# Kernel optimization log

Hardware: AMD Instinct MI355X
Metric: run time of the kernel (lower is better)

The kernel has to match this reference:

```python
import jax, jax.numpy as jnp
import numpy as np

N_NODES = 100000
N_EDGES = 3200000


def setup_inputs() -> dict:
    key = jax.random.key(0)
    ks = jax.random.split(key, 12)
    x = jax.random.normal(ks[0], (N_NODES, 5), dtype=jnp.float32)
    edges = jax.random.randint(ks[1], (2, N_EDGES), 0, N_NODES)
    edge_attr = jax.random.normal(ks[2], (N_EDGES, 2), dtype=jnp.float32)
    detector_labels = jax.random.bernoulli(ks[3], 0.7, (N_NODES,))

    def init(k, shape, fan_in):
        return (jax.random.normal(k, shape, dtype=jnp.float32) / np.sqrt(fan_in)).astype(jnp.float32)

    W_gat = init(ks[4], (5, 16), 5)        # GATConv lin (shared src/dst)
    att_src = init(ks[5], (16,), 16)
    att_dst = init(ks[6], (16,), 16)
    W_edge = init(ks[7], (2, 16), 2)       # GATConv lin_edge
    att_edge = init(ks[8], (16,), 16)
    b_gat = jnp.zeros((16,), jnp.float32)
    W1 = init(ks[9], (34, 64), 34)
    b1 = jnp.zeros((64,), jnp.float32)
    W2 = init(ks[10], (64, 2), 64)
    b2 = jnp.zeros((2,), jnp.float32)
    return dict(x=x, edges=edges, edge_attr=edge_attr, detector_labels=detector_labels,
                W_gat=W_gat, att_src=att_src, att_dst=att_dst, W_edge=W_edge,
                att_edge=att_edge, b_gat=b_gat, W1=W1, b1=b1, W2=W2, b2=b2)


def reference(x, edges, edge_attr, detector_labels, W_gat, att_src, att_dst,
              W_edge, att_edge, b_gat, W1, b1, W2, b2):
    n_nodes = x.shape[0]
    src, dst = edges[0], edges[1]

    # --- GATConv(5 -> 16, heads=1, concat=False, edge_dim=2, no self loops) ---
    h = x @ W_gat                                        # [N, 16]
    a_src = h @ att_src                                  # [N]
    a_dst = h @ att_dst                                  # [N]
    a_edge = (edge_attr @ W_edge) @ att_edge             # [E]
    alpha = jax.nn.leaky_relu(a_src[src] + a_dst[dst] + a_edge, 0.2)
    # segmented softmax over incoming edges of each dst node
    seg_max = jax.ops.segment_max(alpha, dst, num_segments=n_nodes)
    ex = jnp.exp(alpha - seg_max[dst])
    denom = jax.ops.segment_sum(ex, dst, num_segments=n_nodes)
    a = ex / (denom[dst] + 1e-16)                        # [E]
    out = jax.ops.segment_sum(h[src] * a[:, None], dst, num_segments=n_nodes) + b_gat
    xh = jax.nn.relu(out)                                # [N, 16]

    # --- edge update: gather-concat-MLP ---
    feat = jnp.concatenate([xh[src], edge_attr, xh[dst]], axis=-1)   # [E, 34]
    ef = jax.nn.relu(feat @ W1 + b1) @ W2 + b2                       # [E, 2]

    # --- SplitSyndromes: keep edges whose both endpoints are detectors ---
    valid = detector_labels[src] & detector_labels[dst]
    idx = jnp.nonzero(valid)[0]        # eager (data-dependent size, not jitted)
    return edges[:, idx], jax.nn.sigmoid(ef[idx])
```

## Files before the change

kernel.cpp:

```cpp
#include <hip/hip_runtime.h>

#define NN 100000
#define NE 3200000
#define CH 8192
#define NCB ((NE + CH - 1) / CH)
#define THR 1024
#define ITH (CH / THR)
#define NBK ((NN + 63) >> 6)
#define CAP 2560
#define NWG (NE / 64)
#define NSTRIP 8
#define SLEN ((NCB + NSTRIP - 1) / NSTRIP)

typedef __attribute__((ext_vector_type(8))) __bf16 bf16x8;
typedef __attribute__((ext_vector_type(4))) float f32x4;

union BF8 { unsigned short u[8]; bf16x8 v; };

__global__ void kdetect(const unsigned char* __restrict__ lab8, int* __restrict__ flags) {
  __shared__ int tmp[256];
  int t = threadIdx.x;
  int s = 0;
  for (int i = t; i < 25000; i += 256) s += lab8[4 * i + 1];
  tmp[t] = s;
  __syncthreads();
  for (int d = 128; d > 0; d >>= 1) { if (t < d) tmp[t] += tmp[t + d]; __syncthreads(); }
  if (t == 0) flags[0] = (tmp[0] != 0) ? 1 : 0;
}

__global__ void klab(const void* __restrict__ lab, const int* __restrict__ flags,
                     int* __restrict__ labN) {
  int n = blockIdx.x * 256 + threadIdx.x;
  if (n >= NN) return;
  int v;
  if (flags[0]) v = ((const unsigned char*)lab)[n];
  else          v = ((const int*)lab)[n];
  labN[n] = (v != 0) ? 1 : 0;
}

__global__ void kc01(const float* __restrict__ We, const float* __restrict__ ae,
                     float* __restrict__ c01) {
  if (threadIdx.x == 0) {
    float c0 = 0.f, c1 = 0.f;
    for (int k = 0; k < 16; k++) { c0 += We[k] * ae[k]; c1 += We[16 + k] * ae[k]; }
    c01[0] = c0; c01[1] = c1;
  }
}

__global__ void knodeA(const float* __restrict__ x, const float* __restrict__ Wg,
                       const float* __restrict__ atts, const float* __restrict__ attd,
                       const int* __restrict__ labN,
                       float2* __restrict__ pka, float2* __restrict__ pkd) {
  int n = blockIdx.x * 256 + threadIdx.x;
  if (n >= NN) return;
  float xi[5];
#pragma unroll
  for (int i = 0; i < 5; i++) xi[i] = x[n * 5 + i];
  float asum = 0.f, dsum = 0.f;
#pragma unroll
  for (int k = 0; k < 16; k++) {
    float acc = 0.f;
#pragma unroll
    for (int i = 0; i < 5; i++) acc += xi[i] * Wg[i * 16 + k];
    asum += acc * atts[k];
    dsum += acc * attd[k];
  }
  float lab = labN[n] ? 1.f : 0.f;
  pka[n] = make_float2(asum, lab);
  pkd[n] = make_float2(dsum, lab);
}

__global__ __launch_bounds__(THR) void khist(const int* __restrict__ src,
                                             const int* __restrict__ dst,
                                             const int* __restrict__ labN,
                                             int* __restrict__ blkcnt,
                                             int* __restrict__ cntw,
                                             int* __restrict__ cntc) {
  __shared__ int hist[NBK];
  __shared__ int vsum;
  int tid = threadIdx.x, b = blockIdx.x;
  for (int i = tid; i < NBK; i += THR) hist[i] = 0;
  if (tid == 0) vsum = 0;
  __syncthreads();
  int lane = tid & 63, wid = tid >> 6;
  int wsum = 0;
  for (int it = 0; it < ITH; ++it) {
    int e = b * CH + it * THR + tid;
    int v = 0;
    if (e < NE) {
      int s = src[e], d = dst[e];
      atomicAdd(&hist[d >> 6], 1);
      v = labN[s] & labN[d];
    }
    unsigned long long m = __ballot(v != 0);
    int c = __popcll(m);
    if (lane == 0) {
      int wg = b * (CH / 64) + it * 16 + wid;
      if (wg < NWG) cntw[wg] = c;
      wsum += c;
    }
  }
  if (lane == 0) atomicAdd(&vsum, wsum);
  __syncthreads();
  int* row = blkcnt + (size_t)b * NBK;
  for (int i = tid; i < NBK; i += THR) row[i] = hist[i];
  if (tid == 0) cntc[b] = vsum;
}

__global__ __launch_bounds__(256) void kscanc1(int* __restrict__ blkcnt,
                                               int* __restrict__ ssum) {
  int i = blockIdx.x * 256 + threadIdx.x;
  int st = blockIdx.y;
  if (i >= NBK) return;
  int c0 = st * SLEN, c1 = min(c0 + SLEN, NCB);
  int run = 0;
  for (int c = c0; c < c1; c++) {
    int* p = blkcnt + (size_t)c * NBK + i;
    int v = *p;
    *p = run;
    run += v;
  }
  ssum[st * NBK + i] = run;
}

__global__ __launch_bounds__(256) void kscanc2(int* __restrict__ ssum,
                                               int* __restrict__ total) {
  int i = blockIdx.x * 256 + threadIdx.x;
  if (i >= NBK) return;
  int run = 0;
#pragma unroll
  for (int st = 0; st < NSTRIP; st++) {
    int v = ssum[st * NBK + i];
    ssum[st * NBK + i] = run;
    run += v;
  }
  total[i] = run;
}

__global__ __launch_bounds__(256) void kaddbb(int* __restrict__ ssum,
                                              const int* __restrict__ bb) {
  int i = blockIdx.x * 256 + threadIdx.x;
  if (i >= NBK) return;
  int v = bb[i];
#pragma unroll
  for (int st = 0; st < NSTRIP; st++) ssum[st * NBK + i] += v;
}

__global__ void kscan(const int* __restrict__ cnt, int* __restrict__ off, int nb) {
  __shared__ int tmp[256];
  __shared__ int carry;
  int t = threadIdx.x;
  if (t == 0) carry = 0;
  __syncthreads();
  for (int base = 0; base < nb; base += 256) {
    int i = base + t;
    int v = (i < nb) ? cnt[i] : 0;
    tmp[t] = v;
    __syncthreads();
    for (int d = 1; d < 256; d <<= 1) {
      int add = (t >= d) ? tmp[t - d] : 0;
      __syncthreads();
      tmp[t] += add;
      __syncthreads();
    }
    if (i < nb) off[i] = carry + tmp[t] - v;
    __syncthreads();
    if (t == 0) carry += tmp[255];
    __syncthreads();
  }
  if (t == 0) off[nb] = carry;
}

__global__ __launch_bounds__(128) void kscanw(const int* __restrict__ cntw,
                                              const int* __restrict__ offc,
                                              int* __restrict__ offw) {
  int b = blockIdx.x, t = threadIdx.x;
  __shared__ int a[128];
  int wg = b * 128 + t;
  int val = (wg < NWG) ? cntw[wg] : 0;
  a[t] = val;
  __syncthreads();
  for (int d = 1; d < 128; d <<= 1) {
    int x = (t >= d) ? a[t - d] : 0;
    __syncthreads();
    a[t] += x;
    __syncthreads();
  }
  if (wg < NWG) offw[wg] = offc[b] + a[t] - val;
}

__global__ __launch_bounds__(THR) void kscat(
    const int* __restrict__ src, const int* __restrict__ dst,
    const float* __restrict__ eattr,
    const float2* __restrict__ pka, const float2* __restrict__ pkd,
    const float* __restrict__ c01,
    const int* __restrict__ blkcnt, const int* __restrict__ ssum,
    const int* __restrict__ offw,
    uint2* __restrict__ bins, float* __restrict__ out,
    float2* __restrict__ eat2, int NV) {
  __shared__ uint2 pay[CH];
  __shared__ unsigned short pbk[CH];
  __shared__ int hist[2048];
  __shared__ int ps[1024];
  __shared__ int lcur[2048];
  __shared__ int goff[NBK];
  int b = blockIdx.x, tid = threadIdx.x;
  for (int i = tid; i < 2048; i += THR) hist[i] = 0;
  float c0 = c01[0], c1 = c01[1];
  const int* bc = blkcnt + (size_t)b * NBK;
  const int* ss = ssum + (size_t)(b / SLEN) * NBK;
  __syncthreads();
  int lane = tid & 63, wid = tid >> 6;
  uint2 st[ITH];
  unsigned short sb[ITH];
#pragma unroll
  for (int it = 0; it < ITH; ++it) {
    int e = b * CH + it * THR + tid;
    int v = 0;
    int s = 0, d = 0;
    float2 ea;
    if (e < NE) {
      s = src[e]; d = dst[e];
      ea = ((const float2*)eattr)[e];
      float2 ga = pka[s], gd = pkd[d];
      float al = ga.x + gd.x + ea.x * c0 + ea.y * c1;
      al = (al > 0.f) ? al : 0.2f * al;
      float exv = __expf(al);
      int bk = d >> 6;
      atomicAdd(&hist[bk], 1);
      st[it].x = ((unsigned)s << 6) | (unsigned)(d & 63);
      st[it].y = __float_as_uint(exv);
      sb[it] = (unsigned short)bk;
      v = (ga.y != 0.f) && (gd.y != 0.f);
    } else {
      sb[it] = 0xffffu;
    }
    unsigned long long m = __ballot(v);
    if (v) {
      int wg = b * (CH / 64) + it * 16 + wid;
      int p = offw[wg] + __popcll(m & ((1ull << lane) - 1ull));
      if (p < NV) {
        out[p] = (float)s;
        out[NV + p] = (float)d;
        eat2[p] = ea;
      }
    }
  }
  __syncthreads();
  int h0 = hist[2 * tid], h1 = hist[2 * tid + 1];
  ps[tid] = h0 + h1;
  __syncthreads();
  for (int d = 1; d < 1024; d <<= 1) {
    int v = (tid >= d) ? ps[tid - d] : 0;
    __syncthreads();
    ps[tid] += v;
    __syncthreads();
  }
  int epair = (tid > 0) ? ps[tid - 1] : 0;
  int l0 = epair, l1 = epair + h0;
  lcur[2 * tid] = l0;
  lcur[2 * tid + 1] = l1;
  {
    int i0 = 2 * tid, i1 = 2 * tid + 1;
    if (i0 < NBK) goff[i0] = ss[i0] + bc[i0] - l0;
    if (i1 < NBK) goff[i1] = ss[i1] + bc[i1] - l1;
  }
  __syncthreads();
#pragma unroll
  for (int it = 0; it < ITH; ++it) {
    if (sb[it] != 0xffffu) {
      int pos = atomicAdd(&lcur[sb[it]], 1);
      pay[pos] = st[it];
      pbk[pos] = sb[it];
    }
  }
  __syncthreads();
  int n = ps[1023];
  for (int j = tid; j < n; j += THR) {
    int i = pbk[j];
    bins[goff[i] + j] = pay[j];
  }
}

__global__ __launch_bounds__(512) void kagg(
    const uint2* __restrict__ bins, const int* __restrict__ bucket_base,
    const float* __restrict__ x, const float* __restrict__ Wg,
    const float* __restrict__ bg, float* __restrict__ xh) {
  __shared__ uint2 pay[CAP];
  __shared__ int cnt[64], inc[64], cur[64];
  __shared__ float sWg[80], sbg[16];
  int k = blockIdx.x, tid = threadIdx.x;
  if (tid < 80) sWg[tid] = Wg[tid];
  else if (tid < 96) sbg[tid - 80] = bg[tid - 80];
  int start = bucket_base[k], end = bucket_base[k + 1];
  int node0 = k << 6;
  int c = tid & 15, g = tid >> 4;
  __syncthreads();
  float w0 = sWg[c], w1 = sWg[16 + c], w2 = sWg[32 + c], w3 = sWg[48 + c], w4 = sWg[64 + c];
  float acc[2] = {0.f, 0.f}, den[2] = {0.f, 0.f};
  for (int cb = start; cb < end; cb += CAP) {
    int n = min(end - cb, CAP);
    if (tid < 64) cnt[tid] = 0;
    __syncthreads();
    uint2 st0, st1, st2, st3, st4;
    {
      int i;
      i = tid;          if (i < n) { st0 = bins[cb + i]; atomicAdd(&cnt[st0.x & 63], 1); }
      i = tid + 512;    if (i < n) { st1 = bins[cb + i]; atomicAdd(&cnt[st1.x & 63], 1); }
      i = tid + 1024;   if (i < n) { st2 = bins[cb + i]; atomicAdd(&cnt[st2.x & 63], 1); }
      i = tid + 1536;   if (i < n) { st3 = bins[cb + i]; atomicAdd(&cnt[st3.x & 63], 1); }
      i = tid + 2048;   if (i < n) { st4 = bins[cb + i]; atomicAdd(&cnt[st4.x & 63], 1); }
    }
    __syncthreads();
    if (tid < 64) inc[tid] = cnt[tid];
    __syncthreads();
    for (int d = 1; d < 64; d <<= 1) {
      int v = 0;
      if (tid >= d && tid < 64) v = inc[tid - d];
      __syncthreads();
      if (tid < 64) inc[tid] += v;
      __syncthreads();
    }
    if (tid < 64) cur[tid] = inc[tid] - cnt[tid];
    __syncthreads();
    {
      int i;
      i = tid;          if (i < n) pay[atomicAdd(&cur[st0.x & 63], 1)] = st0;
      i = tid + 512;    if (i < n) pay[atomicAdd(&cur[st1.x & 63], 1)] = st1;
      i = tid + 1024;   if (i < n) pay[atomicAdd(&cur[st2.x & 63], 1)] = st2;
      i = tid + 1536;   if (i < n) pay[atomicAdd(&cur[st3.x & 63], 1)] = st3;
      i = tid + 2048;   if (i < n) pay[atomicAdd(&cur[st4.x & 63], 1)] = st4;
    }
    __syncthreads();
#pragma unroll
    for (int p = 0; p < 2; ++p) {
      int nd = p * 32 + g;
      int re = inc[nd], rs = re - cnt[nd];
      float a = 0.f, ds = 0.f;
      for (int idx = rs; idx < re; ++idx) {
        uint2 pl = pay[idx];
        int s = (int)(pl.x >> 6);
        float exv = __uint_as_float(pl.y);
        const float* xp = x + s * 5;
        float h = xp[0] * w0 + xp[1] * w1 + xp[2] * w2 + xp[3] * w3 + xp[4] * w4;
        a += h * exv;
        ds += exv;
      }
      acc[p] += a; den[p] += ds;
    }
    __syncthreads();
  }
#pragma unroll
  for (int p = 0; p < 2; ++p) {
    int node = node0 + p * 32 + g;
    if (node < NN) {
      float dn = fmaxf(den[p], 1e-30f);
      float v = acc[p] / dn + sbg[c];
      xh[node * 16 + c] = (v > 0.f) ? v : 0.f;
    }
  }
}

__global__ __launch_bounds__(256) void kmlp(
    const float2* __restrict__ eat2, const float* __restrict__ xh,
    const float* __restrict__ W1, const float* __restrict__ b1,
    const float* __restrict__ W2, const float* __restrict__ b2,
    float* __restrict__ out, int NV) {
  int tid = threadIdx.x;
  int lane = tid & 63, wid = tid >> 6;
  int lo4 = lane & 15, q = lane >> 4;

  BF8 bh[4], bl[4];
#pragma unroll
  for (int ct = 0; ct < 4; ct++) {
    int col = ct * 16 + lo4;
#pragma unroll
    for (int i = 0; i < 8; i++) {
      int k = q * 8 + i;
      int r = (k < 16) ? k : (k + 2);
      float w = W1[r * 64 + col];
      unsigned u = __float_as_uint(w);
      float rem = w - __uint_as_float(u & 0xffff0000u);
      bh[ct].u[i] = (unsigned short)(u >> 16);
      bl[ct].u[i] = (unsigned short)(__float_as_uint(rem) >> 16);
    }
  }
  float b1v[4], w16v[4], w17v[4], w2a[4], w2b[4];
#pragma unroll
  for (int ct = 0; ct < 4; ct++) {
    int j = ct * 16 + lo4;
    b1v[ct] = b1[j];
    w16v[ct] = W1[16 * 64 + j];
    w17v[ct] = W1[17 * 64 + j];
    w2a[ct] = W2[j * 2 + 0];
    w2b[ct] = W2[j * 2 + 1];
  }
  float bias20 = b2[0], bias21 = b2[1];

  int nwaves = gridDim.x * 4;
  int ntiles = (NV + 15) >> 4;
  for (int tb = blockIdx.x * 4 + wid; tb < ntiles; tb += nwaves) {
    int base = tb * 16;
    BF8 ah, al;
    {
      int p = base + lo4;
      float vals[8] = {0.f, 0.f, 0.f, 0.f, 0.f, 0.f, 0.f, 0.f};
      if (p < NV) {
        int node = (int)out[((q < 2) ? 0 : NV) + p];
        const float4* xp = (const float4*)(xh + node * 16 + (q & 1) * 8);
        float4 f0 = xp[0], f1 = xp[1];
        vals[0] = f0.x; vals[1] = f0.y; vals[2] = f0.z; vals[3] = f0.w;
        vals[4] = f1.x; vals[5] = f1.y; vals[6] = f1.z; vals[7] = f1.w;
      }
#pragma unroll
      for (int i = 0; i < 8; i++) {
        unsigned u = __float_as_uint(vals[i]);
        float rem = vals[i] - __uint_as_float(u & 0xffff0000u);
        ah.u[i] = (unsigned short)(u >> 16);
        al.u[i] = (unsigned short)(__float_as_uint(rem) >> 16);
      }
    }
    f32x4 acc[4];
#pragma unroll
    for (int ct = 0; ct < 4; ct++) {
      f32x4 z = {0.f, 0.f, 0.f, 0.f};
      z = __builtin_amdgcn_mfma_f32_16x16x32_bf16(ah.v, bh[ct].v, z, 0, 0, 0);
      z = __builtin_amdgcn_mfma_f32_16x16x32_bf16(ah.v, bl[ct].v, z, 0, 0, 0);
      z = __builtin_amdgcn_mfma_f32_16x16x32_bf16(al.v, bh[ct].v, z, 0, 0, 0);
      acc[ct] = z;
    }
    float o0[4], o1[4];
#pragma unroll
    for (int reg = 0; reg < 4; reg++) {
      int pr = base + q * 4 + reg;
      float2 ea = make_float2(0.f, 0.f);
      if (pr < NV) ea = eat2[pr];
      float s0 = 0.f, s1 = 0.f;
#pragma unroll
      for (int ct = 0; ct < 4; ct++) {
        float h = acc[ct][reg] + b1v[ct] + ea.x * w16v[ct] + ea.y * w17v[ct];
        h = fmaxf(h, 0.f);
        s0 += h * w2a[ct];
        s1 += h * w2b[ct];
      }
      o0[reg] = s0; o1[reg] = s1;
    }
#pragma unroll
    for (int m = 1; m < 16; m <<= 1) {
#pragma unroll
      for (int reg = 0; reg < 4; reg++) {
        o0[reg] += __shfl_xor(o0[reg], m, 64);
        o1[reg] += __shfl_xor(o1[reg], m, 64);
      }
    }
    if (lo4 == 0) {
#pragma unroll
      for (int reg = 0; reg < 4; reg++) {
        int pr = base + q * 4 + reg;
        if (pr < NV) {
          float v0 = bias20 + o0[reg], v1 = bias21 + o1[reg];
          ((float2*)(out + 2 * (size_t)NV))[pr] = make_float2(
              1.f / (1.f + __expf(-v0)), 1.f / (1.f + __expf(-v1)));
        }
      }
    }
  }
}

static inline size_t al64(size_t v) { return (v + 63) & ~(size_t)63; }

extern "C" void kernel_launch(void* const* d_in, const int* in_sizes, int n_in,
                              void* d_out, int out_size, void* d_ws, size_t ws_size,
                              hipStream_t stream) {
  const float* x     = (const float*)d_in[0];
  const int*   edges = (const int*)d_in[1];
  const float* eattr = (const float*)d_in[2];
  const void*  labels= d_in[3];
  const float* Wg    = (const float*)d_in[4];
  const float* atts  = (const float*)d_in[5];
  const float* attd  = (const float*)d_in[6];
  const float* We    = (const float*)d_in[7];
  const float* atte  = (const float*)d_in[8];
  const float* bg    = (const float*)d_in[9];
  const float* W1    = (const float*)d_in[10];
  const float* b1    = (const float*)d_in[11];
  const float* W2    = (const float*)d_in[12];
  const float* b2    = (const float*)d_in[13];
  float* out = (float*)d_out;
  const int NV = out_size / 4;
  const int* src = edges;
  const int* dst = edges + NE;

  char* w = (char*)d_ws;
  float* xh    = (float*)w;   w += al64((size_t)NN * 64);
  uint2* bins  = (uint2*)w;   w += al64((size_t)NE * 8);
  float2* eat2 = (float2*)w;  w += al64((size_t)NV * 8);
  float2* pka  = (float2*)w;  w += al64((size_t)NN * 8);
  float2* pkd  = (float2*)w;  w += al64((size_t)NN * 8);
  int* labN    = (int*)w;     w += al64((size_t)NN * 4);
  int* blkcnt  = (int*)w;     w += al64((size_t)NCB * NBK * 4);
  int* ssum    = (int*)w;     w += al64((size_t)NSTRIP * NBK * 4);
  int* total   = (int*)w;     w += al64((size_t)NBK * 4);
  int* bb      = (int*)w;     w += al64((size_t)(NBK + 1) * 4);
  int* cntc    = (int*)w;     w += al64((size_t)NCB * 4);
  int* offc    = (int*)w;     w += al64((size_t)(NCB + 1) * 4);
  int* cntw    = (int*)w;     w += al64((size_t)NWG * 4);
  int* offw    = (int*)w;     w += al64((size_t)NWG * 4);
  float* c01   = (float*)w;   w += 64;
  int* flags   = (int*)w;     w += 64;

  kdetect<<<1, 256, 0, stream>>>((const unsigned char*)labels, flags);
  klab<<<(NN + 255) / 256, 256, 0, stream>>>(labels, flags, labN);
  kc01<<<1, 64, 0, stream>>>(We, atte, c01);
  knodeA<<<(NN + 255) / 256, 256, 0, stream>>>(x, Wg, atts, attd, labN, pka, pkd);
  khist<<<NCB, THR, 0, stream>>>(src, dst, labN, blkcnt, cntw, cntc);
  kscanc1<<<dim3((NBK + 255) / 256, NSTRIP), 256, 0, stream>>>(blkcnt, ssum);
  kscanc2<<<(NBK + 255) / 256, 256, 0, stream>>>(ssum, total);
  kscan<<<1, 256, 0, stream>>>(total, bb, NBK);
  kaddbb<<<(NBK + 255) / 256, 256, 0, stream>>>(ssum, bb);
  kscan<<<1, 256, 0, stream>>>(cntc, offc, NCB);
  kscanw<<<NCB, 128, 0, stream>>>(cntw, offc, offw);
  kscat<<<NCB, THR, 0, stream>>>(src, dst, eattr, pka, pkd, c01, blkcnt, ssum,
                                 offw, bins, out, eat2, NV);
  kagg<<<NBK, 512, 0, stream>>>(bins, bb, x, Wg, bg, xh);
  if (NV > 0)
    kmlp<<<2048, 256, 0, stream>>>(eat2, xh, W1, b1, W2, b2, out, NV);
}
```

Before: 280.4 us.

## Store node features pre-split into bf16 hi/lo and pair tiles in MLP

The aggregation kernel now writes each node's features as pre-split bf16 high and low halves, 32 shorts per node, instead of fp32. The MLP kernel then loads the MFMA operands directly, with no per-edge split conversion, and the gathered row is the same 64 bytes. Each wave now handles two 16-edge tiles per iteration for more MFMA and load parallelism. The output reduction is also reworked: each lane folds the two output channels into one value, so the wave needs fewer shuffles, and the two sigmoids are written by different lanes. The costs are higher register pressure and scalar rather than float2 output stores.

```diff
diff --git a/kernel.cpp b/kernel.cpp
--- a/kernel.cpp
+++ b/kernel.cpp
@@ -285,7 +285,7 @@
 __global__ __launch_bounds__(512) void kagg(
     const uint2* __restrict__ bins, const int* __restrict__ bucket_base,
     const float* __restrict__ x, const float* __restrict__ Wg,
-    const float* __restrict__ bg, float* __restrict__ xh) {
+    const float* __restrict__ bg, unsigned short* __restrict__ xb) {
   __shared__ uint2 pay[CAP];
   __shared__ int cnt[64], inc[64], cur[64];
   __shared__ float sWg[80], sbg[16];
@@ -356,13 +356,17 @@
     if (node < NN) {
       float dn = fmaxf(den[p], 1e-30f);
       float v = acc[p] / dn + sbg[c];
-      xh[node * 16 + c] = (v > 0.f) ? v : 0.f;
+      float vv = (v > 0.f) ? v : 0.f;
+      unsigned uv = __float_as_uint(vv);
+      float rem = vv - __uint_as_float(uv & 0xffff0000u);
+      xb[(size_t)node * 32 + c] = (unsigned short)(uv >> 16);
+      xb[(size_t)node * 32 + 16 + c] = (unsigned short)(__float_as_uint(rem) >> 16);
     }
   }
 }
 
 __global__ __launch_bounds__(256) void kmlp(
-    const float2* __restrict__ eat2, const float* __restrict__ xh,
+    const float2* __restrict__ eat2, const unsigned short* __restrict__ xb,
     const float* __restrict__ W1, const float* __restrict__ b1,
     const float* __restrict__ W2, const float* __restrict__ b2,
     float* __restrict__ out, int NV) {
@@ -399,69 +403,82 @@
 
   int nwaves = gridDim.x * 4;
   int ntiles = (NV + 15) >> 4;
-  for (int tb = blockIdx.x * 4 + wid; tb < ntiles; tb += nwaves) {
-    int base = tb * 16;
-    BF8 ah, al;
-    {
-      int p = base + lo4;
-      float vals[8] = {0.f, 0.f, 0.f, 0.f, 0.f, 0.f, 0.f, 0.f};
-      if (p < NV) {
-        int node = (int)out[((q < 2) ? 0 : NV) + p];
-        const float4* xp = (const float4*)(xh + node * 16 + (q & 1) * 8);
-        float4 f0 = xp[0], f1 = xp[1];
-        vals[0] = f0.x; vals[1] = f0.y; vals[2] = f0.z; vals[3] = f0.w;
-        vals[4] = f1.x; vals[5] = f1.y; vals[6] = f1.z; vals[7] = f1.w;
-      }
-#pragma unroll
-      for (int i = 0; i < 8; i++) {
-        unsigned u = __float_as_uint(vals[i]);
-        float rem = vals[i] - __uint_as_float(u & 0xffff0000u);
-        ah.u[i] = (unsigned short)(u >> 16);
-        al.u[i] = (unsigned short)(__float_as_uint(rem) >> 16);
-      }
-    }
-    f32x4 acc[4];
+  int npair = (ntiles + 1) >> 1;
+  const int half = (q < 2) ? 0 : NV;
+  const int hoff = (q & 1) * 8;
+  for (int tp = blockIdx.x * 4 + wid; tp < npair; tp += nwaves) {
+    int baseA = (tp * 2) * 16;
+    int baseB = baseA + 16;
+    int pA = baseA + lo4;
+    int nodeA = (pA < NV) ? (int)out[half + pA] : 0;
+    const unsigned short* xpA = xb + (size_t)nodeA * 32 + hoff;
+    bf16x8 ahA = *(const bf16x8*)xpA;
+    bf16x8 alA = *(const bf16x8*)(xpA + 16);
+    int pB = baseB + lo4;
+    int nodeB = (pB < NV) ? (int)out[half + pB] : 0;
+    const unsigned short* xpB = xb + (size_t)nodeB * 32 + hoff;
+    bf16x8 ahB = *(const bf16x8*)xpB;
+    bf16x8 alB = *(const bf16x8*)(xpB + 16);
+    f32x4 accA[4], accB[4];
 #pragma unroll
     for (int ct = 0; ct < 4; ct++) {
       f32x4 z = {0.f, 0.f, 0.f, 0.f};
-      z = __builtin_amdgcn_mfma_f32_16x16x32_bf16(ah.v, bh[ct].v, z, 0, 0, 0);
-      z = __builtin_amdgcn_mfma_f32_16x16x32_bf16(ah.v, bl[ct].v, z, 0, 0, 0);
-      z = __builtin_amdgcn_mfma_f32_16x16x32_bf16(al.v, bh[ct].v, z, 0, 0, 0);
-      acc[ct] = z;
-    }
-    float o0[4], o1[4];
+      z = __builtin_amdgcn_mfma_f32_16x16x32_bf16(ahA, bh[ct].v, z, 0, 0, 0);
+      z = __builtin_amdgcn_mfma_f32_16x16x32_bf16(ahA, bl[ct].v, z, 0, 0, 0);
+      z = __builtin_amdgcn_mfma_f32_16x16x32_bf16(alA, bh[ct].v, z, 0, 0, 0);
+      accA[ct] = z;
+      f32x4 y = {0.f, 0.f, 0.f, 0.f};
+      y = __builtin_amdgcn_mfma_f32_16x16x32_bf16(ahB, bh[ct].v, y, 0, 0, 0);
+      y = __builtin_amdgcn_mfma_f32_16x16x32_bf16(ahB, bl[ct].v, y, 0, 0, 0);
+      y = __builtin_amdgcn_mfma_f32_16x16x32_bf16(alB, bh[ct].v, y, 0, 0, 0);
+      accB[ct] = y;
+    }
 #pragma unroll
     for (int reg = 0; reg < 4; reg++) {
-      int pr = base + q * 4 + reg;
+      int pr = baseA + q * 4 + reg;
       float2 ea = make_float2(0.f, 0.f);
       if (pr < NV) ea = eat2[pr];
       float s0 = 0.f, s1 = 0.f;
 #pragma unroll
       for (int ct = 0; ct < 4; ct++) {
-        float h = acc[ct][reg] + b1v[ct] + ea.x * w16v[ct] + ea.y * w17v[ct];
+        float h = accA[ct][reg] + b1v[ct] + ea.x * w16v[ct] + ea.y * w17v[ct];
         h = fmaxf(h, 0.f);
         s0 += h * w2a[ct];
         s1 += h * w2b[ct];
       }
-      o0[reg] = s0; o1[reg] = s1;
-    }
-#pragma unroll
-    for (int m = 1; m < 16; m <<= 1) {
-#pragma unroll
-      for (int reg = 0; reg < 4; reg++) {
-        o0[reg] += __shfl_xor(o0[reg], m, 64);
-        o1[reg] += __shfl_xor(o1[reg], m, 64);
+      float a = (lo4 & 8) ? s1 : s0;
+      float g = (lo4 & 8) ? s0 : s1;
+      a += __shfl_xor(g, 8, 64);
+      a += __shfl_xor(a, 4, 64);
+      a += __shfl_xor(a, 2, 64);
+      a += __shfl_xor(a, 1, 64);
+      if (pr < NV) {
+        if (lo4 == 0)      out[2 * (size_t)NV + 2 * pr]     = 1.f / (1.f + __expf(-(bias20 + a)));
+        else if (lo4 == 8) out[2 * (size_t)NV + 2 * pr + 1] = 1.f / (1.f + __expf(-(bias21 + a)));
       }
     }
-    if (lo4 == 0) {
-#pragma unroll
-      for (int reg = 0; reg < 4; reg++) {
-        int pr = base + q * 4 + reg;
-        if (pr < NV) {
-          float v0 = bias20 + o0[reg], v1 = bias21 + o1[reg];
-          ((float2*)(out + 2 * (size_t)NV))[pr] = make_float2(
-              1.f / (1.f + __expf(-v0)), 1.f / (1.f + __expf(-v1)));
-        }
+#pragma unroll
+    for (int reg = 0; reg < 4; reg++) {
+      int pr = baseB + q * 4 + reg;
+      float2 ea = make_float2(0.f, 0.f);
+      if (pr < NV) ea = eat2[pr];
+      float s0 = 0.f, s1 = 0.f;
+#pragma unroll
+      for (int ct = 0; ct < 4; ct++) {
+        float h = accB[ct][reg] + b1v[ct] + ea.x * w16v[ct] + ea.y * w17v[ct];
+        h = fmaxf(h, 0.f);
+        s0 += h * w2a[ct];
+        s1 += h * w2b[ct];
+      }
+      float a = (lo4 & 8) ? s1 : s0;
+      float g = (lo4 & 8) ? s0 : s1;
+      a += __shfl_xor(g, 8, 64);
+      a += __shfl_xor(a, 4, 64);
+      a += __shfl_xor(a, 2, 64);
+      a += __shfl_xor(a, 1, 64);
+      if (pr < NV) {
+        if (lo4 == 0)      out[2 * (size_t)NV + 2 * pr]     = 1.f / (1.f + __expf(-(bias20 + a)));
+        else if (lo4 == 8) out[2 * (size_t)NV + 2 * pr + 1] = 1.f / (1.f + __expf(-(bias21 + a)));
       }
     }
   }
@@ -492,7 +509,7 @@
   const int* dst = edges + NE;
 
   char* w = (char*)d_ws;
-  float* xh    = (float*)w;   w += al64((size_t)NN * 64);
+  unsigned short* xb = (unsigned short*)w;  w += al64((size_t)NN * 64);
   uint2* bins  = (uint2*)w;   w += al64((size_t)NE * 8);
   float2* eat2 = (float2*)w;  w += al64((size_t)NV * 8);
   float2* pka  = (float2*)w;  w += al64((size_t)NN * 8);
@@ -522,7 +539,7 @@
   kscanw<<<NCB, 128, 0, stream>>>(cntw, offc, offw);
   kscat<<<NCB, THR, 0, stream>>>(src, dst, eattr, pka, pkd, c01, blkcnt, ssum,
                                  offw, bins, out, eat2, NV);
-  kagg<<<NBK, 512, 0, stream>>>(bins, bb, x, Wg, bg, xh);
+  kagg<<<NBK, 512, 0, stream>>>(bins, bb, x, Wg, bg, xb);
   if (NV > 0)
-    kmlp<<<2048, 256, 0, stream>>>(eat2, xh, W1, b1, W2, b2, out, NV);
-}
+    kmlp<<<2048, 256, 0, stream>>>(eat2, xb, W1, b1, W2, b2, out, NV);
+}
```

After: 321.2 us. 1.15x slower.
